# Kernel tuning notes

Measured on AMD Instinct MI355X. Metric: run time of the kernel, lower is better.

The kernel has to match this reference:

```python
import jax, jax.numpy as jnp
import numpy as np

B, S, H, E = 4, 2048, 1024, 8

def setup_inputs() -> dict:
    key = jax.random.key(0)
    k1, k2, k3 = jax.random.split(key, 3)
    scale_g = 1.0 / np.sqrt(H)
    scale_e = 1.0 / np.sqrt(H)
    return {
        "x": jax.random.normal(k1, (B, S, H), dtype=jnp.float32),
        "gate_w": jax.random.normal(k2, (H, E), dtype=jnp.float32) * scale_g,
        "gate_b": jnp.zeros((E,), dtype=jnp.float32),
        "expert_w": jax.random.normal(k3, (E, H, H), dtype=jnp.float32) * scale_e,
        "expert_b": jnp.zeros((E, H), dtype=jnp.float32),
    }

def reference(x, gate_w, gate_b, expert_w, expert_b):
    b, s, h = x.shape
    tok = x.reshape(-1, h)                                  # [T, H]
    # gate: softmax over experts per token
    w = jax.nn.softmax(tok @ gate_w + gate_b, axis=-1)      # [T, E]
    # all experts applied to all tokens (dense MoE)
    eo = jnp.einsum("th,ehd->ted", tok, expert_w) + expert_b[None]  # [T, E, H]
    out = jnp.einsum("te,ted->td", w, eo)                   # [T, H]
    return out.reshape(b, s, h)
```

## Files before the change

### kernel.cpp

```cpp
#include <hip/hip_runtime.h>
#include <stdint.h>

typedef unsigned short u16;
typedef short bf8 __attribute__((ext_vector_type(8)));
typedef float f4 __attribute__((ext_vector_type(4)));
typedef _Float16 h2 __attribute__((ext_vector_type(2)));

#define TTOK 8192
#define HD   1024
#define NE   8
#define HH   (HD * HD)

static __device__ __forceinline__ u16 f2bf(float f) {
  union { float f; uint32_t u; } v; v.f = f;
  return (u16)((v.u + 0x7fffu + ((v.u >> 16) & 1u)) >> 16);
}

__global__ __launch_bounds__(256) void gate_conv_kernel(
    const float* __restrict__ x, const float* __restrict__ gw,
    const float* __restrict__ gb, float* __restrict__ wout,
    u16* __restrict__ abf)
{
  const int t    = blockIdx.x * 4 + (threadIdx.x >> 6);
  const int lane = threadIdx.x & 63;
  const float* xr = x + (size_t)t * HD;
  float p[NE];
#pragma unroll
  for (int e = 0; e < NE; ++e) p[e] = 0.f;
#pragma unroll 4
  for (int h = lane; h < HD; h += 64) {
    const float xv = xr[h];
    abf[(size_t)t * HD + h] = f2bf(xv);
    const float* g = gw + (size_t)h * NE;
#pragma unroll
    for (int e = 0; e < NE; ++e) p[e] += xv * g[e];
  }
#pragma unroll
  for (int e = 0; e < NE; ++e) {
#pragma unroll
    for (int off = 32; off > 0; off >>= 1)
      p[e] += __shfl_xor(p[e], off, 64);
    p[e] += gb[e];
  }
  float m = p[0];
#pragma unroll
  for (int e = 1; e < NE; ++e) m = fmaxf(m, p[e]);
  float s = 0.f;
#pragma unroll
  for (int e = 0; e < NE; ++e) { p[e] = expf(p[e] - m); s += p[e]; }
  const float inv = 1.f / s;
  if (lane == 0) {
#pragma unroll
    for (int e = 0; e < NE; ++e) wout[t * NE + e] = p[e] * inv;
  }
}

__global__ __launch_bounds__(256) void wconv_kernel(
    const float* __restrict__ ew, u16* __restrict__ wt)
{
  __shared__ u16 tile[64][66];
  const int e  = blockIdx.z;
  const int h0 = blockIdx.y * 64;
  const int d0 = blockIdx.x * 64;
  const int c  = threadIdx.x & 63;
  const int r0 = threadIdx.x >> 6;
  const float* src = ew + (size_t)e * HH;
  u16* dst = wt + (size_t)e * HH;
#pragma unroll
  for (int i = 0; i < 16; ++i) {
    const int r = i * 4 + r0;
    tile[r][c] = f2bf(src[(size_t)(h0 + r) * HD + d0 + c]);
  }
  __syncthreads();
#pragma unroll
  for (int i = 0; i < 16; ++i) {
    const int r = i * 4 + r0;
    dst[(size_t)(d0 + r) * HD + h0 + c] = tile[c][r];
  }
}

#define BM 256
#define BN 128
#define BK 64
#define SLOT 65536

#define MM(a_, b_, c_) __builtin_amdgcn_mfma_f32_16x16x32_bf16((a_), (b_), (c_), 0, 0, 0)

#define GL(srcp_, dstp_) __builtin_amdgcn_global_load_lds( \
    (const __attribute__((address_space(1))) void*)(srcp_), \
    (__attribute__((address_space(3))) void*)(dstp_), 16, 0, 0)

#define STAGE_A(sq_)                                                \
  {                                                                 \
    const int sk_ = ((sq_) & 15) << 6;                              \
    const u16* as_ = aSrc0 + sk_;                                   \
    char* ad_ = smem + stS + tid * 16;                              \
    GL(as_,          ad_);                                          \
    GL(as_ +  65536, ad_ +  8192);                                  \
    GL(as_ + 131072, ad_ + 16384);                                  \
    GL(as_ + 196608, ad_ + 24576);                                  \
  }
#define STAGE_B(sq_)                                                \
  {                                                                 \
    const int pn_ = (sq_) >> 4;                                     \
    const int sk_ = ((sq_) & 15) << 6;                              \
    const u16* b0_ = bSrc0 + (size_t)(2 * pn_) * HH + sk_;          \
    char* bd_ = smem + stS + 32768 + tid * 16;                      \
    GL(b0_,          bd_);                                          \
    GL(b0_ +  65536, bd_ +  8192);                                  \
    GL(b0_ + HH,          bd_ + 16384);                             \
    GL(b0_ + HH + 65536,  bd_ + 24576);                             \
  }

#define MFMA16E(ACC_, A0_, A1_, A2_, A3_, B0_, B1_, B2_, B3_)  \
    ACC_[0][0] = MM(A0_, B0_, ACC_[0][0]);                     \
    ACC_[1][0] = MM(A1_, B0_, ACC_[1][0]);                     \
    ACC_[2][0] = MM(A2_, B0_, ACC_[2][0]);                     \
    ACC_[3][0] = MM(A3_, B0_, ACC_[3][0]);                     \
    ACC_[0][1] = MM(A0_, B1_, ACC_[0][1]);                     \
    ACC_[1][1] = MM(A1_, B1_, ACC_[1][1]);                     \
    ACC_[2][1] = MM(A2_, B1_, ACC_[2][1]);                     \
    ACC_[3][1] = MM(A3_, B1_, ACC_[3][1]);                     \
    ACC_[0][2] = MM(A0_, B2_, ACC_[0][2]);                     \
    ACC_[1][2] = MM(A1_, B2_, ACC_[1][2]);                     \
    ACC_[2][2] = MM(A2_, B2_, ACC_[2][2]);                     \
    ACC_[3][2] = MM(A3_, B2_, ACC_[3][2]);                     \
    ACC_[0][3] = MM(A0_, B3_, ACC_[0][3]);                     \
    ACC_[1][3] = MM(A1_, B3_, ACC_[1][3]);                     \
    ACC_[2][3] = MM(A3 == A3 ? A3_ : A3_, B3_, ACC_[2][3]);    \
    ACC_[3][3] = MM(A3_, B3_, ACC_[3][3]);

#undef MFMA16E
#define MFMA16E(ACC_, A0_, A1_, A2_, A3_, B0_, B1_, B2_, B3_)  \
    ACC_[0][0] = MM(A0_, B0_, ACC_[0][0]);                     \
    ACC_[1][0] = MM(A1_, B0_, ACC_[1][0]);                     \
    ACC_[2][0] = MM(A2_, B0_, ACC_[2][0]);                     \
    ACC_[3][0] = MM(A3_, B0_, ACC_[3][0]);                     \
    ACC_[0][1] = MM(A0_, B1_, ACC_[0][1]);                     \
    ACC_[1][1] = MM(A1_, B1_, ACC_[1][1]);                     \
    ACC_[2][1] = MM(A2_, B1_, ACC_[2][1]);                     \
    ACC_[3][1] = MM(A3_, B1_, ACC_[3][1]);                     \
    ACC_[0][2] = MM(A0_, B2_, ACC_[0][2]);                     \
    ACC_[1][2] = MM(A1_, B2_, ACC_[1][2]);                     \
    ACC_[2][2] = MM(A2_, B2_, ACC_[2][2]);                     \
    ACC_[3][2] = MM(A3_, B2_, ACC_[3][2]);                     \
    ACC_[0][3] = MM(A0_, B3_, ACC_[0][3]);                     \
    ACC_[1][3] = MM(A1_, B3_, ACC_[1][3]);                     \
    ACC_[2][3] = MM(A2_, B3_, ACC_[2][3]);                     \
    ACC_[3][3] = MM(A3_, B3_, ACC_[3][3]);

#define FOLD(e0_, e1_)                                                  \
  {                                                                     \
    _Pragma("unroll")                                                   \
    for (int mi = 0; mi < 4; ++mi) {                                    \
      const int r_ = wrb + mi * 16 + lhi * 4;                           \
      float wa[4], wb[4];                                               \
      _Pragma("unroll")                                                 \
      for (int j = 0; j < 4; ++j) {                                     \
        wa[j] = wgs[(r_ + j) * 9 + (e0_)];                              \
        wb[j] = wgs[(r_ + j) * 9 + (e1_)];                              \
      }                                                                 \
      _Pragma("unroll")                                                 \
      for (int ni = 0; ni < 4; ++ni) {                                  \
        const float f0 = wa[0] * acc0[mi][ni][0] + wb[0] * acc1[mi][ni][0]; \
        const float f1 = wa[1] * acc0[mi][ni][1] + wb[1] * acc1[mi][ni][1]; \
        const float f2 = wa[2] * acc0[mi][ni][2] + wb[2] * acc1[mi][ni][2]; \
        const float f3 = wa[3] * acc0[mi][ni][3] + wb[3] * acc1[mi][ni][3]; \
        h2 t0; t0[0] = (_Float16)f0; t0[1] = (_Float16)f1;              \
        h2 t1; t1[0] = (_Float16)f2; t1[1] = (_Float16)f3;              \
        accP0[mi][ni] += t0;                                            \
        accP1[mi][ni] += t1;                                            \
        acc0[mi][ni] = fz; acc1[mi][ni] = fz;                           \
      }                                                                 \
    }                                                                   \
  }

#define BAR       __builtin_amdgcn_s_barrier();
#define VM0       asm volatile("s_waitcnt vmcnt(0)" ::: "memory");
#define LGKM(n_)  asm volatile("s_waitcnt lgkmcnt(" #n_ ")" ::: "memory");
#define SCHED0    __builtin_amdgcn_sched_barrier(0);
#define PRIO1     __builtin_amdgcn_s_setprio(1);
#define PRIO0     __builtin_amdgcn_s_setprio(0);

#define TILE_BODY(DO_STAGE_, sq_)                                        \
  {                                                                      \
    const char* aP0 = smem + curS + thrA0;                               \
    const char* aP1 = smem + curS + thrA1;                               \
    const char* bP0 = smem + curS + thrB0;                               \
    const char* bP1 = smem + curS + thrB1;                               \
                                       \
    bf8 a00 = *(const bf8*)(aP0);                                        \
    bf8 a01 = *(const bf8*)(aP0 + 2048);                                 \
    bf8 a02 = *(const bf8*)(aP0 + 4096);                                 \
    bf8 a03 = *(const bf8*)(aP0 + 6144);                                 \
    bf8 b000 = *(const bf8*)(bP0);                                       \
    bf8 b001 = *(const bf8*)(bP0 + 2048);                                \
    bf8 b002 = *(const bf8*)(bP0 + 4096);                                \
    bf8 b003 = *(const bf8*)(bP0 + 6144);                                \
                          \
    bf8 b100 = *(const bf8*)(bP0 + 16384);                               \
    bf8 b101 = *(const bf8*)(bP0 + 18432);                               \
    bf8 b102 = *(const bf8*)(bP0 + 20480);                               \
    bf8 b103 = *(const bf8*)(bP0 + 22528);                               \
    if (DO_STAGE_) STAGE_A(sq_)                                          \
    LGKM(4) SCHED0                                                       \
    PRIO1 MFMA16E(acc0, a00, a01, a02, a03, b000, b001, b002, b003)      \
    PRIO0 SCHED0                                                         \
              \
    bf8 a10 = *(const bf8*)(aP1);                                        \
    bf8 a11 = *(const bf8*)(aP1 + 2048);                                 \
    bf8 a12 = *(const bf8*)(aP1 + 4096);                                 \
    bf8 a13 = *(const bf8*)(aP1 + 6144);                                 \
    bf8 b010 = *(const bf8*)(bP1);                                       \
    bf8 b011 = *(const bf8*)(bP1 + 2048);                                \
    bf8 b012 = *(const bf8*)(bP1 + 4096);                                \
    bf8 b013 = *(const bf8*)(bP1 + 6144);                                \
    LGKM(8) SCHED0                                                       \
    PRIO1 MFMA16E(acc1, a00, a01, a02, a03, b100, b101, b102, b103)      \
    PRIO0 SCHED0                                                         \
    if (DO_STAGE_) STAGE_B(sq_)                                          \
                          \
    bf8 b110 = *(const bf8*)(bP1 + 16384);                               \
    bf8 b111 = *(const bf8*)(bP1 + 18432);                               \
    bf8 b112 = *(const bf8*)(bP1 + 20480);                               \
    bf8 b113 = *(const bf8*)(bP1 + 22528);                               \
    LGKM(4) SCHED0                                                       \
    PRIO1 MFMA16E(acc0, a10, a11, a12, a13, b010, b011, b012, b013)      \
    PRIO0 SCHED0                                                         \
    LGKM(0) SCHED0                                                       \
    PRIO1 MFMA16E(acc1, a10, a11, a12, a13, b110, b111, b112, b113)      \
    PRIO0 SCHED0                                                         \
  }

__global__ __launch_bounds__(512, 2) void moe_gemm_kernel(
    const u16* __restrict__ A,
    const u16* __restrict__ Wt,
    const float* __restrict__ wg,
    const float* __restrict__ eb,
    float* __restrict__ out)
{
  __shared__ __attribute__((aligned(16))) char smem[2 * SLOT + 9216];
  float* wgs = (float*)(smem + 2 * SLOT);

  const int bid   = blockIdx.x;
  const int xcd   = bid & 7;
  const int local = bid >> 3;
  const int bm    = xcd * 4 + (local & 3);
  const int bn    = local >> 2;
  const int row0  = bm * BM;
  const int col0  = bn * BN;

  const int tid  = threadIdx.x;
  const int lane = tid & 63;
  const int wid  = tid >> 6;
  const int wr   = wid >> 1;
  const int wc   = wid & 1;
  const int l15  = lane & 15;
  const int lhi  = lane >> 4;
  const int wrb  = wr * 64;
  const int wcb  = wc * 64;

  const int gsl   = (lhi ^ (l15 & 7)) << 4;
  const int thrA0 = wrb * 128 + l15 * 128 + gsl;
  const int thrA1 = thrA0 ^ 64;
  const int thrB0 = 32768 + wcb * 128 + l15 * 128 + gsl;
  const int thrB1 = thrB0 ^ 64;

  const int row_in = tid >> 3;
  const int gsw    = (tid & 7) ^ (row_in & 7);
  const u16* aSrc0 = A  + (size_t)(row0 + row_in) * HD + gsw * 8;
  const u16* bSrc0 = Wt + (size_t)(col0 + row_in) * HD + gsw * 8;

  {
    const f4 v = *(const f4*)(wg + (size_t)row0 * NE + tid * 4);
    const int i0 = tid * 4;
#pragma unroll
    for (int k = 0; k < 4; ++k) {
      const int idx = i0 + k;
      wgs[(idx >> 3) * 9 + (idx & 7)] = v[k];
    }
  }
  LGKM(0)

  const f4 fz = {0.f, 0.f, 0.f, 0.f};
  const h2 hz = {(_Float16)0.f, (_Float16)0.f};
  f4 acc0[4][4], acc1[4][4];
  h2 accP0[4][4], accP1[4][4];
#pragma unroll
  for (int i = 0; i < 4; ++i)
#pragma unroll
    for (int j = 0; j < 4; ++j) {
      acc0[i][j] = fz; acc1[i][j] = fz;
      accP0[i][j] = hz; accP1[i][j] = hz;
    }

  int curS = 0, stS = SLOT;

  { const int sv = stS; stS = 0; STAGE_A(0) STAGE_B(0) stS = sv; }

  for (int q = 0; q < 63; ++q) {
    VM0
    BAR
    TILE_BODY(1, q + 1)
    { const int t_ = curS; curS = stS; stS = t_; }
    if ((q & 15) == 15) { const int p_ = q >> 4; FOLD(2 * p_, 2 * p_ + 1) }
  }
  VM0
  BAR
  TILE_BODY(0, 0)
  FOLD(6, 7)

  float ebv[4][8];
#pragma unroll
  for (int ni = 0; ni < 4; ++ni) {
    const int d = col0 + wcb + ni * 16 + l15;
#pragma unroll
    for (int e2 = 0; e2 < NE; ++e2) ebv[ni][e2] = eb[(size_t)e2 * HD + d];
  }
#pragma unroll
  for (int mi = 0; mi < 4; ++mi) {
    const int r_ = wrb + mi * 16 + lhi * 4;
#pragma unroll
    for (int j = 0; j < 4; ++j) {
      const int t = row0 + r_ + j;
      const float* wrow = &wgs[(r_ + j) * 9];
#pragma unroll
      for (int ni = 0; ni < 4; ++ni) {
        const float bias =
            wrow[0] * ebv[ni][0] + wrow[1] * ebv[ni][1] +
            wrow[2] * ebv[ni][2] + wrow[3] * ebv[ni][3] +
            wrow[4] * ebv[ni][4] + wrow[5] * ebv[ni][5] +
            wrow[6] * ebv[ni][6] + wrow[7] * ebv[ni][7];
        const float v = (j < 2) ? (float)accP0[mi][ni][j & 1]
                                : (float)accP1[mi][ni][j & 1];
        const int d = col0 + wcb + ni * 16 + l15;
        out[(size_t)t * HD + d] = v + bias;
      }
    }
  }
}

extern "C" void kernel_launch(void* const* d_in, const int* in_sizes, int n_in,
                              void* d_out, int out_size, void* d_ws, size_t ws_size,
                              hipStream_t stream) {
  const float* x  = (const float*)d_in[0];
  const float* gw = (const float*)d_in[1];
  const float* gb = (const float*)d_in[2];
  const float* ew = (const float*)d_in[3];
  const float* eb = (const float*)d_in[4];
  float* out = (float*)d_out;

  char* ws = (char*)d_ws;
  u16*   abf   = (u16*)ws;
  u16*   wt    = (u16*)(ws + (size_t)16 * 1024 * 1024);
  float* wgate = (float*)(ws + (size_t)32 * 1024 * 1024);

  gate_conv_kernel<<<dim3(TTOK / 4), dim3(256), 0, stream>>>(x, gw, gb, wgate, abf);
  wconv_kernel<<<dim3(16, 16, 8), dim3(256), 0, stream>>>(ew, wt);
  moe_gemm_kernel<<<dim3((TTOK / BM) * (HD / BN)), dim3(512), 0, stream>>>(abf, wt, wgate, eb, out);
}
```

Measured before the change: 135.4 us.

## Load A fragments directly to registers and ring-buffer B in four LDS slots

```diff
diff --git a/kernel.cpp b/kernel.cpp
--- a/kernel.cpp
+++ b/kernel.cpp
@@ -82,7 +82,7 @@
 #define BM 256
 #define BN 128
 #define BK 64
-#define SLOT 65536
+#define SLOTB 32768
 
 #define MM(a_, b_, c_) __builtin_amdgcn_mfma_f32_16x16x32_bf16((a_), (b_), (c_), 0, 0, 0)
 
@@ -90,47 +90,31 @@
     (const __attribute__((address_space(1))) void*)(srcp_), \
     (__attribute__((address_space(3))) void*)(dstp_), 16, 0, 0)
 
-#define STAGE_A(sq_)                                                \
-  {                                                                 \
-    const int sk_ = ((sq_) & 15) << 6;                              \
-    const u16* as_ = aSrc0 + sk_;                                   \
-    char* ad_ = smem + stS + tid * 16;                              \
-    GL(as_,          ad_);                                          \
-    GL(as_ +  65536, ad_ +  8192);                                  \
-    GL(as_ + 131072, ad_ + 16384);                                  \
-    GL(as_ + 196608, ad_ + 24576);                                  \
-  }
-#define STAGE_B(sq_)                                                \
-  {                                                                 \
-    const int pn_ = (sq_) >> 4;                                     \
-    const int sk_ = ((sq_) & 15) << 6;                              \
-    const u16* b0_ = bSrc0 + (size_t)(2 * pn_) * HH + sk_;          \
-    char* bd_ = smem + stS + 32768 + tid * 16;                      \
-    GL(b0_,          bd_);                                          \
-    GL(b0_ +  65536, bd_ +  8192);                                  \
-    GL(b0_ + HH,          bd_ + 16384);                             \
-    GL(b0_ + HH + 65536,  bd_ + 24576);                             \
-  }
-
-#define MFMA16E(ACC_, A0_, A1_, A2_, A3_, B0_, B1_, B2_, B3_)  \
-    ACC_[0][0] = MM(A0_, B0_, ACC_[0][0]);                     \
-    ACC_[1][0] = MM(A1_, B0_, ACC_[1][0]);                     \
-    ACC_[2][0] = MM(A2_, B0_, ACC_[2][0]);                     \
-    ACC_[3][0] = MM(A3_, B0_, ACC_[3][0]);                     \
-    ACC_[0][1] = MM(A0_, B1_, ACC_[0][1]);                     \
-    ACC_[1][1] = MM(A1_, B1_, ACC_[1][1]);                     \
-    ACC_[2][1] = MM(A2_, B1_, ACC_[2][1]);                     \
-    ACC_[3][1] = MM(A3_, B1_, ACC_[3][1]);                     \
-    ACC_[0][2] = MM(A0_, B2_, ACC_[0][2]);                     \
-    ACC_[1][2] = MM(A1_, B2_, ACC_[1][2]);                     \
-    ACC_[2][2] = MM(A2_, B2_, ACC_[2][2]);                     \
-    ACC_[3][2] = MM(A3_, B2_, ACC_[3][2]);                     \
-    ACC_[0][3] = MM(A0_, B3_, ACC_[0][3]);                     \
-    ACC_[1][3] = MM(A1_, B3_, ACC_[1][3]);                     \
-    ACC_[2][3] = MM(A3 == A3 ? A3_ : A3_, B3_, ACC_[2][3]);    \
-    ACC_[3][3] = MM(A3_, B3_, ACC_[3][3]);
-
-#undef MFMA16E
+#define STAGE_B(sq_)                                                 \
+  {                                                                  \
+    const int pn_ = (sq_) >> 4;                                      \
+    const int sk_ = ((sq_) & 15) << 6;                               \
+    const u16* b0_ = bSrc0 + (size_t)(2 * pn_) * HH + sk_;           \
+    char* bd_ = smem + ((sq_) & 3) * SLOTB + tid * 16;               \
+    GL(b0_,          bd_);                                           \
+    GL(b0_ +  65536, bd_ +  8192);                                   \
+    GL(b0_ + HH,          bd_ + 16384);                              \
+    GL(b0_ + HH + 65536,  bd_ + 24576);                              \
+  }
+
+#define LOAD_A(NB_, aq_)                                             \
+  {                                                                  \
+    const char* ap_ = aBase + ((((aq_) & 15)) << 7);                 \
+    aF[NB_][0][0] = *(const bf8*)(ap_);                              \
+    aF[NB_][0][1] = *(const bf8*)(ap_ + 64);                         \
+    aF[NB_][1][0] = *(const bf8*)(ap_ + 32768);                      \
+    aF[NB_][1][1] = *(const bf8*)(ap_ + 32832);                      \
+    aF[NB_][2][0] = *(const bf8*)(ap_ + 65536);                      \
+    aF[NB_][2][1] = *(const bf8*)(ap_ + 65600);                      \
+    aF[NB_][3][0] = *(const bf8*)(ap_ + 98304);                      \
+    aF[NB_][3][1] = *(const bf8*)(ap_ + 98368);                      \
+  }
+
 #define MFMA16E(ACC_, A0_, A1_, A2_, A3_, B0_, B1_, B2_, B3_)  \
     ACC_[0][0] = MM(A0_, B0_, ACC_[0][0]);                     \
     ACC_[1][0] = MM(A1_, B0_, ACC_[1][0]);                     \
@@ -176,60 +160,51 @@
   }
 
 #define BAR       __builtin_amdgcn_s_barrier();
-#define VM0       asm volatile("s_waitcnt vmcnt(0)" ::: "memory");
 #define LGKM(n_)  asm volatile("s_waitcnt lgkmcnt(" #n_ ")" ::: "memory");
 #define SCHED0    __builtin_amdgcn_sched_barrier(0);
 #define PRIO1     __builtin_amdgcn_s_setprio(1);
 #define PRIO0     __builtin_amdgcn_s_setprio(0);
 
-#define TILE_BODY(DO_STAGE_, sq_)                                        \
+#define TILE(q_, CB_, NB_, DO_A_, DO_ST_, VMN_)                          \
   {                                                                      \
-    const char* aP0 = smem + curS + thrA0;                               \
-    const char* aP1 = smem + curS + thrA1;                               \
-    const char* bP0 = smem + curS + thrB0;                               \
-    const char* bP1 = smem + curS + thrB1;                               \
-                                       \
-    bf8 a00 = *(const bf8*)(aP0);                                        \
-    bf8 a01 = *(const bf8*)(aP0 + 2048);                                 \
-    bf8 a02 = *(const bf8*)(aP0 + 4096);                                 \
-    bf8 a03 = *(const bf8*)(aP0 + 6144);                                 \
-    bf8 b000 = *(const bf8*)(bP0);                                       \
-    bf8 b001 = *(const bf8*)(bP0 + 2048);                                \
-    bf8 b002 = *(const bf8*)(bP0 + 4096);                                \
-    bf8 b003 = *(const bf8*)(bP0 + 6144);                                \
-                          \
-    bf8 b100 = *(const bf8*)(bP0 + 16384);                               \
-    bf8 b101 = *(const bf8*)(bP0 + 18432);                               \
-    bf8 b102 = *(const bf8*)(bP0 + 20480);                               \
-    bf8 b103 = *(const bf8*)(bP0 + 22528);                               \
-    if (DO_STAGE_) STAGE_A(sq_)                                          \
-    LGKM(4) SCHED0                                                       \
-    PRIO1 MFMA16E(acc0, a00, a01, a02, a03, b000, b001, b002, b003)      \
-    PRIO0 SCHED0                                                         \
-              \
-    bf8 a10 = *(const bf8*)(aP1);                                        \
-    bf8 a11 = *(const bf8*)(aP1 + 2048);                                 \
-    bf8 a12 = *(const bf8*)(aP1 + 4096);                                 \
-    bf8 a13 = *(const bf8*)(aP1 + 6144);                                 \
-    bf8 b010 = *(const bf8*)(bP1);                                       \
-    bf8 b011 = *(const bf8*)(bP1 + 2048);                                \
-    bf8 b012 = *(const bf8*)(bP1 + 4096);                                \
-    bf8 b013 = *(const bf8*)(bP1 + 6144);                                \
-    LGKM(8) SCHED0                                                       \
-    PRIO1 MFMA16E(acc1, a00, a01, a02, a03, b100, b101, b102, b103)      \
-    PRIO0 SCHED0                                                         \
-    if (DO_STAGE_) STAGE_B(sq_)                                          \
-                          \
-    bf8 b110 = *(const bf8*)(bP1 + 16384);                               \
-    bf8 b111 = *(const bf8*)(bP1 + 18432);                               \
-    bf8 b112 = *(const bf8*)(bP1 + 20480);                               \
-    bf8 b113 = *(const bf8*)(bP1 + 22528);                               \
-    LGKM(4) SCHED0                                                       \
-    PRIO1 MFMA16E(acc0, a10, a11, a12, a13, b010, b011, b012, b013)      \
-    PRIO0 SCHED0                                                         \
-    LGKM(0) SCHED0                                                       \
-    PRIO1 MFMA16E(acc1, a10, a11, a12, a13, b110, b111, b112, b113)      \
-    PRIO0 SCHED0                                                         \
+    asm volatile("s_waitcnt vmcnt(" #VMN_ ")" ::: "memory");             \
+    BAR                                                                  \
+    const char* bQ0 = smem + ((q_) & 3) * SLOTB + thrB0;                 \
+    const char* bQ1 = smem + ((q_) & 3) * SLOTB + thrB1;                 \
+    {                                                                    \
+      bf8 b00 = *(const bf8*)(bQ0);                                      \
+      bf8 b01 = *(const bf8*)(bQ0 + 2048);                               \
+      bf8 b02 = *(const bf8*)(bQ0 + 4096);                               \
+      bf8 b03 = *(const bf8*)(bQ0 + 6144);                               \
+      bf8 b10 = *(const bf8*)(bQ0 + 16384);                              \
+      bf8 b11 = *(const bf8*)(bQ0 + 18432);                              \
+      bf8 b12 = *(const bf8*)(bQ0 + 20480);                              \
+      bf8 b13 = *(const bf8*)(bQ0 + 22528);                              \
+      if (DO_A_) LOAD_A(NB_, (q_) + 1)                                   \
+      if (DO_ST_) STAGE_B((q_) + 3)                                      \
+      LGKM(4) SCHED0                                                     \
+      PRIO1 MFMA16E(acc0, aF[CB_][0][0], aF[CB_][1][0], aF[CB_][2][0],   \
+                    aF[CB_][3][0], b00, b01, b02, b03) PRIO0 SCHED0      \
+      LGKM(0) SCHED0                                                     \
+      PRIO1 MFMA16E(acc1, aF[CB_][0][0], aF[CB_][1][0], aF[CB_][2][0],   \
+                    aF[CB_][3][0], b10, b11, b12, b13) PRIO0 SCHED0      \
+    }                                                                    \
+    {                                                                    \
+      bf8 b00 = *(const bf8*)(bQ1);                                      \
+      bf8 b01 = *(const bf8*)(bQ1 + 2048);                               \
+      bf8 b02 = *(const bf8*)(bQ1 + 4096);                               \
+      bf8 b03 = *(const bf8*)(bQ1 + 6144);                               \
+      bf8 b10 = *(const bf8*)(bQ1 + 16384);                              \
+      bf8 b11 = *(const bf8*)(bQ1 + 18432);                              \
+      bf8 b12 = *(const bf8*)(bQ1 + 20480);                              \
+      bf8 b13 = *(const bf8*)(bQ1 + 22528);                              \
+      LGKM(4) SCHED0                                                     \
+      PRIO1 MFMA16E(acc0, aF[CB_][0][1], aF[CB_][1][1], aF[CB_][2][1],   \
+                    aF[CB_][3][1], b00, b01, b02, b03) PRIO0 SCHED0      \
+      LGKM(0) SCHED0                                                     \
+      PRIO1 MFMA16E(acc1, aF[CB_][0][1], aF[CB_][1][1], aF[CB_][2][1],   \
+                    aF[CB_][3][1], b10, b11, b12, b13) PRIO0 SCHED0      \
+    }                                                                    \
   }
 
 __global__ __launch_bounds__(512, 2) void moe_gemm_kernel(
@@ -239,8 +214,8 @@
     const float* __restrict__ eb,
     float* __restrict__ out)
 {
-  __shared__ __attribute__((aligned(16))) char smem[2 * SLOT + 9216];
-  float* wgs = (float*)(smem + 2 * SLOT);
+  __shared__ __attribute__((aligned(16))) char smem[4 * SLOTB + 9216];
+  float* wgs = (float*)(smem + 4 * SLOTB);
 
   const int bid   = blockIdx.x;
   const int xcd   = bid & 7;
@@ -261,15 +236,14 @@
   const int wcb  = wc * 64;
 
   const int gsl   = (lhi ^ (l15 & 7)) << 4;
-  const int thrA0 = wrb * 128 + l15 * 128 + gsl;
-  const int thrA1 = thrA0 ^ 64;
-  const int thrB0 = 32768 + wcb * 128 + l15 * 128 + gsl;
+  const int thrB0 = wcb * 128 + l15 * 128 + gsl;
   const int thrB1 = thrB0 ^ 64;
 
   const int row_in = tid >> 3;
   const int gsw    = (tid & 7) ^ (row_in & 7);
-  const u16* aSrc0 = A  + (size_t)(row0 + row_in) * HD + gsw * 8;
   const u16* bSrc0 = Wt + (size_t)(col0 + row_in) * HD + gsw * 8;
+
+  const char* aBase = (const char*)A + ((size_t)(row0 + wrb + l15) << 11) + lhi * 16;
 
   {
     const f4 v = *(const f4*)(wg + (size_t)row0 * NE + tid * 4);
@@ -286,6 +260,7 @@
   const h2 hz = {(_Float16)0.f, (_Float16)0.f};
   f4 acc0[4][4], acc1[4][4];
   h2 accP0[4][4], accP1[4][4];
+  bf8 aF[2][4][2];
 #pragma unroll
   for (int i = 0; i < 4; ++i)
 #pragma unroll
@@ -294,20 +269,18 @@
       accP0[i][j] = hz; accP1[i][j] = hz;
     }
 
-  int curS = 0, stS = SLOT;
-
-  { const int sv = stS; stS = 0; STAGE_A(0) STAGE_B(0) stS = sv; }
-
-  for (int q = 0; q < 63; ++q) {
-    VM0
-    BAR
-    TILE_BODY(1, q + 1)
-    { const int t_ = curS; curS = stS; stS = t_; }
-    if ((q & 15) == 15) { const int p_ = q >> 4; FOLD(2 * p_, 2 * p_ + 1) }
-  }
-  VM0
-  BAR
-  TILE_BODY(0, 0)
+  LOAD_A(0, 0)
+  STAGE_B(0) STAGE_B(1) STAGE_B(2)
+
+  for (int q = 0; q < 60; q += 2) {
+    TILE(q,     0, 1, 1, 1, 4)
+    TILE(q + 1, 1, 0, 1, 1, 4)
+    if ((q & 15) == 14) { const int p_ = q >> 4; FOLD(2 * p_, 2 * p_ + 1) }
+  }
+  TILE(60, 0, 1, 1, 1, 0)
+  TILE(61, 1, 0, 1, 0, 0)
+  TILE(62, 0, 1, 1, 0, 0)
+  TILE(63, 1, 0, 0, 0, 0)
   FOLD(6, 7)
 
   float ebv[4][8];
```

New measurement: 212.1 us. +56.6%, slower.
